# Kernel tuning notes

Measured on AMD Instinct MI355X. Metric: run time of the kernel, lower is better.

## Reference

```python
import jax, jax.numpy as jnp
import numpy as np

N_PTS = 32768      # n_x == n_y (query points == source points)
K_NBR = 32         # neighbors per query point
N_EDGES = N_PTS * K_NBR
D_COORD = 3
C = 64             # f_y channels == MLP output channels
H = 256            # MLP hidden width


def setup_inputs() -> dict:
    key = jax.random.key(0)
    ks = jax.random.split(key, 12)
    y = jax.random.normal(ks[0], (N_PTS, D_COORD), dtype=jnp.float32)
    x = jax.random.normal(ks[1], (N_PTS, D_COORD), dtype=jnp.float32)
    f_y = jax.random.normal(ks[2], (N_PTS, C), dtype=jnp.float32)
    neighbors_index = jax.random.randint(ks[3], (N_EDGES,), 0, N_PTS, dtype=jnp.int64)
    neighbors_row_splits = (jnp.arange(N_PTS + 1, dtype=jnp.int64) * K_NBR)
    weights = jax.random.uniform(ks[4], (N_EDGES,), dtype=jnp.float32)
    # LinearChannelMLP params: layers [6, 256, 256, 64], gelu between layers
    def dense(k, fan_in, fan_out):
        w = jax.random.normal(k, (fan_in, fan_out), dtype=jnp.float32) / np.sqrt(fan_in)
        return w
    W0 = dense(ks[5], 2 * D_COORD, H)
    b0 = jnp.zeros((H,), dtype=jnp.float32)
    W1 = dense(ks[6], H, H)
    b1 = jnp.zeros((H,), dtype=jnp.float32)
    W2 = dense(ks[7], H, C)
    b2 = jnp.zeros((C,), dtype=jnp.float32)
    return {"y": y, "x": x, "f_y": f_y,
            "neighbors_index": neighbors_index,
            "neighbors_row_splits": neighbors_row_splits,
            "weights": weights,
            "W0": W0, "b0": b0, "W1": W1, "b1": b1, "W2": W2, "b2": b2}


def reference(y, x, f_y, neighbors_index, neighbors_row_splits, weights,
              W0, b0, W1, b1, W2, b2):
    n_x = neighbors_row_splits.shape[0] - 1
    n_edges = neighbors_index.shape[0]
    # CSR row id for each edge (equivalent to repeat(arange(n_x), num_reps))
    seg = jnp.searchsorted(neighbors_row_splits, jnp.arange(n_edges), side='right') - 1
    rep_features = y[neighbors_index]            # [E, 3] gathered source coords
    self_features = x[seg]                       # [E, 3] repeated query coords
    agg = jnp.concatenate([rep_features, self_features], axis=-1)  # [E, 6]
    # channel MLP (gelu between layers, none after last)
    h = jax.nn.gelu(agg @ W0 + b0)
    h = jax.nn.gelu(h @ W1 + b1)
    rep = h @ W2 + b2                            # [E, C] kernel values
    # transform_type='linear': kernel * f_y(neighbor)
    rep = rep * f_y[neighbors_index]
    # quadrature weights (forces sum reduction, as in source)
    rep = rep * weights[:, None]
    out = jax.ops.segment_sum(rep, seg, num_segments=n_x)  # segment-CSR sum
    return out
```

## Files before the change

### kernel.cpp

```cpp
#include <hip/hip_runtime.h>
#include <hip/hip_bf16.h>
#include <stdint.h>

#define NPTS 32768
#define KNBR 32
#define NEDGES (NPTS * KNBR)
#define TM 128
#define AGG_STRIDE 40
#define H_STRIDE 264

typedef __attribute__((ext_vector_type(8))) short short8;
typedef __attribute__((ext_vector_type(4))) float f32x4;
typedef __attribute__((ext_vector_type(4))) unsigned int u32x4;
typedef __attribute__((ext_vector_type(2))) unsigned int u32x2;

__device__ __forceinline__ unsigned short f2bf(float f) {
    unsigned int u = __float_as_uint(f);
    unsigned int r = (u + 0x7FFFu + ((u >> 16) & 1u)) >> 16;
    return (unsigned short)r;
}

__device__ __forceinline__ unsigned int cvt_pk_bf16(float lo, float hi) {
    unsigned int r;
    asm("v_cvt_pk_bf16_f32 %0, %1, %2" : "=v"(r) : "v"(lo), "v"(hi));
    return r;
}

__device__ __forceinline__ float gelu_tanh(float x) {
    float x2 = x * x;
    float u = fmaf(-0.102942496f, x2, -2.30220824f);
    float e = __builtin_amdgcn_exp2f(x * u);
    return x * __builtin_amdgcn_rcpf(1.0f + e);
}

__global__ void pack_w(const float* __restrict__ W0, const float* __restrict__ W1,
                       const float* __restrict__ W2, unsigned short* __restrict__ wp) {
    int tid = blockIdx.x * blockDim.x + threadIdx.x;
    if (tid >= 176 * 64) return;
    int fid = tid >> 6, l = tid & 63, ln = l & 15, lg = l >> 4;
    unsigned short v[8];
    if (fid < 16) {
        int nt = fid, k0 = lg * 8;
        #pragma unroll
        for (int j = 0; j < 8; ++j) {
            int k = k0 + j;
            v[j] = f2bf(k < 6 ? W0[k * 256 + nt * 16 + ln] : 0.0f);
        }
    } else if (fid < 144) {
        int g = fid - 16;
        int nt = g >> 3, s = g & 7;
        int col = nt * 16 + ln;
        int k0 = s * 32 + lg * 8;
        #pragma unroll
        for (int j = 0; j < 8; ++j) v[j] = f2bf(W1[(k0 + j) * 256 + col]);
    } else {
        int g = fid - 144;
        int c = g >> 3, s = g & 7;
        int col = c * 16 + ln;
        int k0 = s * 32 + lg * 8;
        #pragma unroll
        for (int j = 0; j < 8; ++j) v[j] = f2bf(W2[(k0 + j) * 64 + col]);
    }
    unsigned short* o = &wp[tid * 8];
    #pragma unroll
    for (int j = 0; j < 8; ++j) o[j] = v[j];
}

__global__ __launch_bounds__(512, 3)
void gno_fused(const float* __restrict__ y, const float* __restrict__ x,
               const float* __restrict__ f_y, const int* __restrict__ nbr,
               const float* __restrict__ wts,
               const float* __restrict__ b0, const float* __restrict__ b1,
               const float* __restrict__ b2,
               const unsigned short* __restrict__ wp,
               float* __restrict__ out) {
    __shared__ __align__(16) unsigned short agg_lds[TM * AGG_STRIDE];
    __shared__ __align__(16) unsigned short h_lds[TM * H_STRIDE];

    const int b = blockIdx.x;
    const int tid = threadIdx.x;
    const int l = tid & 63;
    const int w = tid >> 6;
    const int wm = w & 1;
    const int wn = w >> 1;
    const int lg = l >> 4;
    const int ln = l & 15;
    const int ebase = b * TM;

    const char* wpb = (const char*)wp;
    const char* pW0 = wpb + wn * 4096 + l * 16;
    const char* pW1 = wpb + 16384 + wn * 32768 + l * 16;
    const char* pW2 = wpb + 147456 + wn * 8192 + l * 16;
    const char* aggb = (const char*)agg_lds + ln * 80 + lg * 16;
    char* hwb = (char*)h_lds + ln * 528 + wn * 128 + lg * 8;
    const char* hrb = (const char*)h_lds + ln * 528 + lg * 16;

    if (tid < TM) {
        int e = ebase + tid;
        int j = nbr[e];
        int i = e >> 5;
        const float* yr = &y[j * 3];
        const float* xr = &x[i * 3];
        u32x4 q0;
        q0.x = cvt_pk_bf16(yr[0], yr[1]);
        q0.y = cvt_pk_bf16(yr[2], xr[0]);
        q0.z = cvt_pk_bf16(xr[1], xr[2]);
        q0.w = 0u;
        u32x4 z = {0u, 0u, 0u, 0u};
        unsigned short* row = &agg_lds[tid * AGG_STRIDE];
        *(u32x4*)(row +  0) = q0;
        *(u32x4*)(row +  8) = z;
        *(u32x4*)(row + 16) = z;
        *(u32x4*)(row + 24) = z;
    }
    __syncthreads();

    {
        short8 ag[4];
        #pragma unroll
        for (int mt = 0; mt < 4; ++mt)
            ag[mt] = *(const short8*)(aggb + (4 * wm + mt) * 1280);
        #pragma unroll
        for (int q = 0; q < 4; ++q) {
            short8 aw = *(const short8*)(pW0 + q * 1024);
            f32x4 b0f = *(const f32x4*)&b0[(4 * wn + q) * 16 + lg * 4];
            #pragma unroll
            for (int mt = 0; mt < 4; ++mt) {
                f32x4 c = __builtin_amdgcn_mfma_f32_16x16x32_bf16(aw, ag[mt], b0f, 0, 0, 0);
                u32x2 pv;
                pv.x = cvt_pk_bf16(gelu_tanh(c[0]), gelu_tanh(c[1]));
                pv.y = cvt_pk_bf16(gelu_tanh(c[2]), gelu_tanh(c[3]));
                *(u32x2*)(hwb + (4 * wm + mt) * 8448 + q * 32) = pv;
            }
        }
    }
    __syncthreads();

    f32x4 acc[4][4];
    #pragma unroll
    for (int q = 0; q < 4; ++q) {
        f32x4 b1f = *(const f32x4*)&b1[(4 * wn + q) * 16 + lg * 4];
        #pragma unroll
        for (int mt = 0; mt < 4; ++mt) acc[mt][q] = b1f;
    }
    #pragma unroll 2
    for (int s = 0; s < 8; ++s) {
        short8 hb[4];
        #pragma unroll
        for (int mt = 0; mt < 4; ++mt)
            hb[mt] = *(const short8*)(hrb + (4 * wm + mt) * 8448 + s * 64);
        #pragma unroll
        for (int q = 0; q < 4; ++q) {
            short8 aw = *(const short8*)(pW1 + q * 8192 + s * 1024);
            #pragma unroll
            for (int mt = 0; mt < 4; ++mt)
                acc[mt][q] = __builtin_amdgcn_mfma_f32_16x16x32_bf16(aw, hb[mt], acc[mt][q], 0, 0, 0);
        }
    }
    __syncthreads();

    #pragma unroll
    for (int q = 0; q < 4; ++q) {
        #pragma unroll
        for (int mt = 0; mt < 4; ++mt) {
            u32x2 pv;
            pv.x = cvt_pk_bf16(gelu_tanh(acc[mt][q][0]), gelu_tanh(acc[mt][q][1]));
            pv.y = cvt_pk_bf16(gelu_tanh(acc[mt][q][2]), gelu_tanh(acc[mt][q][3]));
            *(u32x2*)(hwb + (4 * wm + mt) * 8448 + q * 32) = pv;
        }
    }
    __syncthreads();

    f32x4 fy[4];
    float wv[4];
    #pragma unroll
    for (int m = 0; m < 4; ++m) {
        int e = ebase + (wm * 4 + m) * 16 + ln;
        int j = nbr[e];
        fy[m] = *(const f32x4*)&f_y[j * 64 + wn * 16 + lg * 4];
        wv[m] = wts[e];
    }

    f32x4 acc3[4];
    {
        f32x4 b2f = *(const f32x4*)&b2[wn * 16 + lg * 4];
        #pragma unroll
        for (int m = 0; m < 4; ++m) acc3[m] = b2f;
    }
    const char* hrb3 = hrb + wm * 33792;
    #pragma unroll 2
    for (int s = 0; s < 8; ++s) {
        short8 aw = *(const short8*)(pW2 + s * 1024);
        #pragma unroll
        for (int m = 0; m < 4; ++m) {
            short8 hb = *(const short8*)(hrb3 + m * 8448 + s * 64);
            acc3[m] = __builtin_amdgcn_mfma_f32_16x16x32_bf16(aw, hb, acc3[m], 0, 0, 0);
        }
    }

    {
        f32x4 seg[2];
        seg[0] = (f32x4){0.f, 0.f, 0.f, 0.f};
        seg[1] = (f32x4){0.f, 0.f, 0.f, 0.f};
        #pragma unroll
        for (int m = 0; m < 4; ++m) {
            f32x4 v;
            #pragma unroll
            for (int i = 0; i < 4; ++i)
                v[i] = acc3[m][i] * fy[m][i] * wv[m];
            seg[m >> 1] += v;
        }
        #pragma unroll
        for (int g = 0; g < 2; ++g) {
            f32x4 v = seg[g];
            #pragma unroll
            for (int d = 1; d <= 8; d <<= 1) {
                #pragma unroll
                for (int i = 0; i < 4; ++i)
                    v[i] += __shfl_xor(v[i], d, 64);
            }
            if (ln == 0)
                *(f32x4*)&out[(b * 4 + wm * 2 + g) * 64 + wn * 16 + lg * 4] = v;
        }
    }
}

extern "C" void kernel_launch(void* const* d_in, const int* in_sizes, int n_in,
                              void* d_out, int out_size, void* d_ws, size_t ws_size,
                              hipStream_t stream) {
    const float* y   = (const float*)d_in[0];
    const float* x   = (const float*)d_in[1];
    const float* f_y = (const float*)d_in[2];
    const int*   nbr = (const int*)d_in[3];
    const float* wts = (const float*)d_in[5];
    const float* W0  = (const float*)d_in[6];
    const float* b0  = (const float*)d_in[7];
    const float* W1  = (const float*)d_in[8];
    const float* b1  = (const float*)d_in[9];
    const float* W2  = (const float*)d_in[10];
    const float* b2  = (const float*)d_in[11];
    unsigned short* wp = (unsigned short*)d_ws;
    float* out = (float*)d_out;

    pack_w<<<dim3(44), dim3(256), 0, stream>>>(W0, W1, W2, wp);
    gno_fused<<<dim3(NEDGES / TM), dim3(512), 0, stream>>>(
        y, x, f_y, nbr, wts, b0, b1, b2, wp, out);
}
```

Measured before the change: 288.1 us.

## Halve edge tile to 64 with 256-thread blocks and pack GELU math

The edge tile per block drops from 128 to 64 and the block from 8 waves to 4, so each wave covers all 64 edges and one 64-column slice of the hidden layer, and the M-direction wave split is removed. This halves LDS per block and raises the occupancy hint to 4 blocks per CU, aiming for more latency hiding. GELU is rewritten on 2-wide float vectors so the compiler can emit packed FP32 ops. The cost is twice as many blocks and twice as many weight fragment loads per edge, since each block now reads the full weight set for half as many edges.

```diff
diff --git a/kernel.cpp b/kernel.cpp
--- a/kernel.cpp
+++ b/kernel.cpp
@@ -5,12 +5,13 @@
 #define NPTS 32768
 #define KNBR 32
 #define NEDGES (NPTS * KNBR)
-#define TM 128
+#define TM 64
 #define AGG_STRIDE 40
 #define H_STRIDE 264
 
 typedef __attribute__((ext_vector_type(8))) short short8;
 typedef __attribute__((ext_vector_type(4))) float f32x4;
+typedef __attribute__((ext_vector_type(2))) float f32x2;
 typedef __attribute__((ext_vector_type(4))) unsigned int u32x4;
 typedef __attribute__((ext_vector_type(2))) unsigned int u32x2;
 
@@ -26,11 +27,27 @@
     return r;
 }
 
-__device__ __forceinline__ float gelu_tanh(float x) {
-    float x2 = x * x;
-    float u = fmaf(-0.102942496f, x2, -2.30220824f);
-    float e = __builtin_amdgcn_exp2f(x * u);
-    return x * __builtin_amdgcn_rcpf(1.0f + e);
+__device__ __forceinline__ f32x2 gelu2v(f32x2 x) {
+    f32x2 x2 = x * x;
+    f32x2 u = x2 * (-0.102942496f) + (f32x2){-2.30220824f, -2.30220824f};
+    f32x2 t = x * u;
+    f32x2 e;
+    e.x = __builtin_amdgcn_exp2f(t.x);
+    e.y = __builtin_amdgcn_exp2f(t.y);
+    f32x2 d = e + 1.0f;
+    f32x2 r;
+    r.x = __builtin_amdgcn_rcpf(d.x);
+    r.y = __builtin_amdgcn_rcpf(d.y);
+    return x * r;
+}
+
+__device__ __forceinline__ u32x2 gelu4_pk(f32x4 c) {
+    f32x2 g01 = gelu2v((f32x2){c[0], c[1]});
+    f32x2 g23 = gelu2v((f32x2){c[2], c[3]});
+    u32x2 pv;
+    pv.x = cvt_pk_bf16(g01.x, g01.y);
+    pv.y = cvt_pk_bf16(g23.x, g23.y);
+    return pv;
 }
 
 __global__ void pack_w(const float* __restrict__ W0, const float* __restrict__ W1,
@@ -66,7 +83,7 @@
     for (int j = 0; j < 8; ++j) o[j] = v[j];
 }
 
-__global__ __launch_bounds__(512, 3)
+__global__ __launch_bounds__(256, 4)
 void gno_fused(const float* __restrict__ y, const float* __restrict__ x,
                const float* __restrict__ f_y, const int* __restrict__ nbr,
                const float* __restrict__ wts,
@@ -81,18 +98,16 @@
     const int tid = threadIdx.x;
     const int l = tid & 63;
     const int w = tid >> 6;
-    const int wm = w & 1;
-    const int wn = w >> 1;
     const int lg = l >> 4;
     const int ln = l & 15;
     const int ebase = b * TM;
 
     const char* wpb = (const char*)wp;
-    const char* pW0 = wpb + wn * 4096 + l * 16;
-    const char* pW1 = wpb + 16384 + wn * 32768 + l * 16;
-    const char* pW2 = wpb + 147456 + wn * 8192 + l * 16;
+    const char* pW0 = wpb + w * 4096 + l * 16;
+    const char* pW1 = wpb + 16384 + w * 32768 + l * 16;
+    const char* pW2 = wpb + 147456 + w * 8192 + l * 16;
     const char* aggb = (const char*)agg_lds + ln * 80 + lg * 16;
-    char* hwb = (char*)h_lds + ln * 528 + wn * 128 + lg * 8;
+    char* hwb = (char*)h_lds + ln * 528 + w * 128 + lg * 8;
     const char* hrb = (const char*)h_lds + ln * 528 + lg * 16;
 
     if (tid < TM) {
@@ -119,18 +134,15 @@
         short8 ag[4];
         #pragma unroll
         for (int mt = 0; mt < 4; ++mt)
-            ag[mt] = *(const short8*)(aggb + (4 * wm + mt) * 1280);
+            ag[mt] = *(const short8*)(aggb + mt * 1280);
         #pragma unroll
         for (int q = 0; q < 4; ++q) {
             short8 aw = *(const short8*)(pW0 + q * 1024);
-            f32x4 b0f = *(const f32x4*)&b0[(4 * wn + q) * 16 + lg * 4];
+            f32x4 b0f = *(const f32x4*)&b0[(4 * w + q) * 16 + lg * 4];
             #pragma unroll
             for (int mt = 0; mt < 4; ++mt) {
                 f32x4 c = __builtin_amdgcn_mfma_f32_16x16x32_bf16(aw, ag[mt], b0f, 0, 0, 0);
-                u32x2 pv;
-                pv.x = cvt_pk_bf16(gelu_tanh(c[0]), gelu_tanh(c[1]));
-                pv.y = cvt_pk_bf16(gelu_tanh(c[2]), gelu_tanh(c[3]));
-                *(u32x2*)(hwb + (4 * wm + mt) * 8448 + q * 32) = pv;
+                *(u32x2*)(hwb + mt * 8448 + q * 32) = gelu4_pk(c);
             }
         }
     }
@@ -139,7 +151,7 @@
     f32x4 acc[4][4];
     #pragma unroll
     for (int q = 0; q < 4; ++q) {
-        f32x4 b1f = *(const f32x4*)&b1[(4 * wn + q) * 16 + lg * 4];
+        f32x4 b1f = *(const f32x4*)&b1[(4 * w + q) * 16 + lg * 4];
         #pragma unroll
         for (int mt = 0; mt < 4; ++mt) acc[mt][q] = b1f;
     }
@@ -148,7 +160,7 @@
         short8 hb[4];
         #pragma unroll
         for (int mt = 0; mt < 4; ++mt)
-            hb[mt] = *(const short8*)(hrb + (4 * wm + mt) * 8448 + s * 64);
+            hb[mt] = *(const short8*)(hrb + mt * 8448 + s * 64);
         #pragma unroll
         for (int q = 0; q < 4; ++q) {
             short8 aw = *(const short8*)(pW1 + q * 8192 + s * 1024);
@@ -163,10 +175,7 @@
     for (int q = 0; q < 4; ++q) {
         #pragma unroll
         for (int mt = 0; mt < 4; ++mt) {
-            u32x2 pv;
-            pv.x = cvt_pk_bf16(gelu_tanh(acc[mt][q][0]), gelu_tanh(acc[mt][q][1]));
-            pv.y = cvt_pk_bf16(gelu_tanh(acc[mt][q][2]), gelu_tanh(acc[mt][q][3]));
-            *(u32x2*)(hwb + (4 * wm + mt) * 8448 + q * 32) = pv;
+            *(u32x2*)(hwb + mt * 8448 + q * 32) = gelu4_pk(acc[mt][q]);
         }
     }
     __syncthreads();
@@ -175,25 +184,24 @@
     float wv[4];
     #pragma unroll
     for (int m = 0; m < 4; ++m) {
-        int e = ebase + (wm * 4 + m) * 16 + ln;
+        int e = ebase + m * 16 + ln;
         int j = nbr[e];
-        fy[m] = *(const f32x4*)&f_y[j * 64 + wn * 16 + lg * 4];
+        fy[m] = *(const f32x4*)&f_y[j * 64 + w * 16 + lg * 4];
         wv[m] = wts[e];
     }
 
     f32x4 acc3[4];
     {
-        f32x4 b2f = *(const f32x4*)&b2[wn * 16 + lg * 4];
+        f32x4 b2f = *(const f32x4*)&b2[w * 16 + lg * 4];
         #pragma unroll
         for (int m = 0; m < 4; ++m) acc3[m] = b2f;
     }
-    const char* hrb3 = hrb + wm * 33792;
     #pragma unroll 2
     for (int s = 0; s < 8; ++s) {
         short8 aw = *(const short8*)(pW2 + s * 1024);
         #pragma unroll
         for (int m = 0; m < 4; ++m) {
-            short8 hb = *(const short8*)(hrb3 + m * 8448 + s * 64);
+            short8 hb = *(const short8*)(hrb + m * 8448 + s * 64);
             acc3[m] = __builtin_amdgcn_mfma_f32_16x16x32_bf16(aw, hb, acc3[m], 0, 0, 0);
         }
     }
@@ -220,7 +228,7 @@
                     v[i] += __shfl_xor(v[i], d, 64);
             }
             if (ln == 0)
-                *(f32x4*)&out[(b * 4 + wm * 2 + g) * 64 + wn * 16 + lg * 4] = v;
+                *(f32x4*)&out[(2 * b + g) * 64 + w * 16 + lg * 4] = v;
         }
     }
 }
@@ -243,6 +251,6 @@
     float* out = (float*)d_out;
 
     pack_w<<<dim3(44), dim3(256), 0, stream>>>(W0, W1, W2, wp);
-    gno_fused<<<dim3(NEDGES / TM), dim3(512), 0, stream>>>(
+    gno_fused<<<dim3(NEDGES / TM), dim3(256), 0, stream>>>(
         y, x, f_y, nbr, wts, b0, b1, b2, wp, out);
 }
```

After: 270.5 us. 1.07x faster.
